# Optimization experiments

Measured on AMD Instinct MI355X. Metric: run time of the kernel, lower is better.

Reference implementation:

```python
import jax, jax.numpy as jnp
import numpy as np

N_HEADS = 16

def setup_inputs() -> dict:
    key = jax.random.key(0)
    ks = jax.random.split(key, 6)
    B, S, D = 2, 2048, 1024
    return {
        "hidden_states": jax.random.normal(ks[0], (B, S, D), dtype=jnp.float32),
        "Wq": jax.random.normal(ks[1], (D, D), dtype=jnp.float32) * (1.0 / np.sqrt(D)),
        "Wk": jax.random.normal(ks[2], (D, D), dtype=jnp.float32) * (1.0 / np.sqrt(D)),
        "Wv": jax.random.normal(ks[3], (D, D), dtype=jnp.float32) * (1.0 / np.sqrt(D)),
        "Wo": jax.random.normal(ks[4], (D, D), dtype=jnp.float32) * (1.0 / np.sqrt(D)),
        "bo": jnp.zeros((D,), dtype=jnp.float32),
    }

def reference(hidden_states, Wq, Wk, Wv, Wo, bo):
    B, S, D = hidden_states.shape
    H = N_HEADS
    hd = D // H  # head_dim; d_kv == d_model per module's final view
    # nn.Linear(bias=False): x @ W.T, then the module's direct view to (B, H, S, hd)
    q = (hidden_states @ Wq.T).reshape(B, H, S, hd)
    k = (hidden_states @ Wk.T).reshape(B, H, S, hd)  # self-attention path (encoder_states=None)
    v = (hidden_states @ Wv.T).reshape(B, H, S, hd)
    # naive full score matrix [B, H, S, S]
    wei = jnp.einsum('bhqd,bhkd->bhqk', q, k)
    causal = jnp.tril(jnp.ones((S, S), dtype=bool))
    wei = jnp.where(causal, wei, -jnp.inf)
    # NOTE: module divides logits by head_dim (not sqrt) -- preserved faithfully
    attn = jax.nn.softmax(wei / hd, axis=-1)
    ctx = jnp.einsum('bhqk,bhkd->bhqd', attn, v)  # [B, H, S, hd]
    out = ctx.transpose(0, 2, 1, 3).reshape(B, S, D)
    return out @ Wo.T + bo
```

## Files before the change

### kernel.cpp

```cpp
#include <hip/hip_runtime.h>

#define S_LEN   2048
#define D_MODEL 1024
#define N_HEADS 16
#define HEAD_DIM 64

typedef unsigned short u16;
typedef float  floatx4 __attribute__((ext_vector_type(4)));
typedef short  bf16x8  __attribute__((ext_vector_type(8)));
typedef short  bf16x4  __attribute__((ext_vector_type(4)));

__device__ __forceinline__ u16 f2bf(float f) {
    unsigned int u = __float_as_uint(f);
    u += 0x7FFF + ((u >> 16) & 1);
    return (u16)(u >> 16);
}
__device__ __forceinline__ unsigned pack2bf(float a, float b) {
    return (unsigned)f2bf(a) | ((unsigned)f2bf(b) << 16);
}

__device__ __forceinline__ void gload_lds16(const void* g, void* l) {
    __builtin_amdgcn_global_load_lds(
        reinterpret_cast<const __attribute__((address_space(1))) unsigned int*>(
            reinterpret_cast<uintptr_t>(g)),
        reinterpret_cast<__attribute__((address_space(3))) unsigned int*>(
            reinterpret_cast<uintptr_t>(l)),
        16, 0, 0);
}

__global__ __launch_bounds__(256) void cast_all(const float* __restrict__ hs,
                                                const float* __restrict__ w0,
                                                const float* __restrict__ w1,
                                                const float* __restrict__ w2,
                                                const float* __restrict__ w3,
                                                u16* __restrict__ dst) {
    const size_t NHS = (size_t)2 * S_LEN * D_MODEL;
    const size_t e0 = (size_t)blockIdx.x * 2048;
    const float* src;
    size_t base;
    if (e0 < NHS)                 { src = hs; base = 0; }
    else {
        const int wi = (int)((e0 - NHS) >> 20);
        src = wi == 0 ? w0 : wi == 1 ? w1 : wi == 2 ? w2 : w3;
        base = NHS + ((size_t)wi << 20);
    }
    const size_t i = e0 + (size_t)threadIdx.x * 8;
    const float4 a = *(const float4*)(src + (i - base));
    const float4 b = *(const float4*)(src + (i - base) + 4);
    uint4 o;
    o.x = pack2bf(a.x, a.y); o.y = pack2bf(a.z, a.w);
    o.z = pack2bf(b.x, b.y); o.w = pack2bf(b.z, b.w);
    *(uint4*)(dst + i) = o;
}

__global__ __launch_bounds__(256) void vtrans(const u16* __restrict__ Vf,
                                              u16* __restrict__ Vt) {
    __shared__ unsigned T[64 * 133];
    const int bh = blockIdx.y;
    const int sBase = blockIdx.x * 128;
    const u16* src = Vf + (size_t)bh * (S_LEN * HEAD_DIM) + (size_t)sBase * HEAD_DIM;
    u16* dst = Vt + (size_t)bh * (S_LEN * HEAD_DIM) + sBase;
    const int tid = threadIdx.x;

#pragma unroll
    for (int it = 0; it < 4; ++it) {
        const int idx = it * 256 + tid;
        const int row = idx >> 3, ch = idx & 7;
        const float4 v4 = *(const float4*)(src + row * 64 + ch * 8);
        const u16* vs = (const u16*)&v4;
#pragma unroll
        for (int j = 0; j < 8; ++j) T[(ch * 8 + j) * 133 + row] = vs[j];
    }
    __syncthreads();
#pragma unroll
    for (int it = 0; it < 4; ++it) {
        const int idx = it * 256 + tid;
        const int d = idx >> 4, sc = idx & 15;
        union { u16 u[8]; float4 f; } tmp;
#pragma unroll
        for (int j = 0; j < 8; ++j) tmp.u[j] = (u16)T[d * 133 + sc * 8 + j];
        *(float4*)(dst + (size_t)d * S_LEN + sc * 8) = tmp.f;
    }
}

__global__ __launch_bounds__(256) void gemm_qkv(const u16* __restrict__ A,
                                                const u16* __restrict__ Wq,
                                                const u16* __restrict__ Wk,
                                                const u16* __restrict__ Wv,
                                                u16* __restrict__ Qo,
                                                u16* __restrict__ Ko,
                                                u16* __restrict__ Vfo) {
    __shared__ u16 As[8 * 512];
    __shared__ u16 Ws[8 * 512];

    const int blk = blockIdx.x;
    const int y   = (blk & 7) | (((blk >> 3) & 3) << 3);
    const int x   = blk >> 5;
    const int which = x >> 3;
    const int nBase = (x & 7) * 128;
    const int mBase = y * 128;
    const u16* W = which == 0 ? Wq : which == 1 ? Wk : Wv;

    const int tid = threadIdx.x, lane = tid & 63, wv = tid >> 6;
    const int l15 = lane & 15, quad = lane >> 4;
    const int wm = wv & 1, wn = wv >> 1;
    const int srow = lane >> 2;
    const int gch  = (lane & 3) ^ ((lane >> 3) & 3);
    const int swz  = (l15 >> 1) & 3;

    floatx4 acc[4][4];
#pragma unroll
    for (int i = 0; i < 4; ++i)
#pragma unroll
        for (int j = 0; j < 4; ++j) acc[i][j] = (floatx4)(0.0f);

    for (int k0 = 0; k0 < D_MODEL; k0 += 32) {
        __syncthreads();
#pragma unroll
        for (int t = 0; t < 2; ++t) {
            const int ci = wv * 2 + t;
            gload_lds16(A + (size_t)(mBase + ci * 16 + srow) * D_MODEL + k0 + gch * 8,
                        &As[ci * 512]);
            gload_lds16(W + (size_t)(nBase + ci * 16 + srow) * D_MODEL + k0 + gch * 8,
                        &Ws[ci * 512]);
        }
        __syncthreads();

        bf16x8 af[4], bfr[4];
#pragma unroll
        for (int mt = 0; mt < 4; ++mt)
            af[mt] = *(const bf16x8*)&As[(wm * 64 + mt * 16 + l15) * 32 + (quad ^ swz) * 8];
#pragma unroll
        for (int nt = 0; nt < 4; ++nt)
            bfr[nt] = *(const bf16x8*)&Ws[(wn * 64 + nt * 16 + l15) * 32 + (quad ^ swz) * 8];
#pragma unroll
        for (int mt = 0; mt < 4; ++mt)
#pragma unroll
            for (int nt = 0; nt < 4; ++nt)
                acc[mt][nt] = __builtin_amdgcn_mfma_f32_16x16x32_bf16(af[mt], bfr[nt], acc[mt][nt], 0, 0, 0);
    }

    u16* O = which == 0 ? Qo : (which == 1 ? Ko : Vfo);
    const float scale = which == 0 ? (1.44269504088896f / 64.0f) : 1.0f;
#pragma unroll
    for (int mt = 0; mt < 4; ++mt)
#pragma unroll
        for (int nt = 0; nt < 4; ++nt) {
            const int col = nBase + wn * 64 + nt * 16 + l15;
#pragma unroll
            for (int r = 0; r < 4; ++r) {
                const int row = mBase + wm * 64 + mt * 16 + quad * 4 + r;
                O[(size_t)row * D_MODEL + col] = f2bf(acc[mt][nt][r] * scale);
            }
        }
}

__global__ __launch_bounds__(256) void gemm_out(const u16* __restrict__ A,
                                                const u16* __restrict__ W,
                                                const float* __restrict__ bias,
                                                float* __restrict__ C) {
    __shared__ u16 As[4 * 512];
    __shared__ u16 Ws[8 * 512];

    const int nBase = blockIdx.x * 128;
    const int mBase = blockIdx.y * 64;
    const int tid = threadIdx.x, lane = tid & 63, wv = tid >> 6;
    const int l15 = lane & 15, quad = lane >> 4;
    const int wm = wv & 1, wn = wv >> 1;
    const int srow = lane >> 2;
    const int gch  = (lane & 3) ^ ((lane >> 3) & 3);
    const int swz  = (l15 >> 1) & 3;

    floatx4 acc[2][4];
#pragma unroll
    for (int i = 0; i < 2; ++i)
#pragma unroll
        for (int j = 0; j < 4; ++j) acc[i][j] = (floatx4)(0.0f);

    for (int k0 = 0; k0 < D_MODEL; k0 += 32) {
        __syncthreads();
        gload_lds16(A + (size_t)(mBase + wv * 16 + srow) * D_MODEL + k0 + gch * 8,
                    &As[wv * 512]);
#pragma unroll
        for (int t = 0; t < 2; ++t) {
            const int ci = wv * 2 + t;
            gload_lds16(W + (size_t)(nBase + ci * 16 + srow) * D_MODEL + k0 + gch * 8,
                        &Ws[ci * 512]);
        }
        __syncthreads();

        bf16x8 af[2], bfr[4];
#pragma unroll
        for (int mt = 0; mt < 2; ++mt)
            af[mt] = *(const bf16x8*)&As[(wm * 32 + mt * 16 + l15) * 32 + (quad ^ swz) * 8];
#pragma unroll
        for (int nt = 0; nt < 4; ++nt)
            bfr[nt] = *(const bf16x8*)&Ws[(wn * 64 + nt * 16 + l15) * 32 + (quad ^ swz) * 8];
#pragma unroll
        for (int mt = 0; mt < 2; ++mt)
#pragma unroll
            for (int nt = 0; nt < 4; ++nt)
                acc[mt][nt] = __builtin_amdgcn_mfma_f32_16x16x32_bf16(af[mt], bfr[nt], acc[mt][nt], 0, 0, 0);
    }

#pragma unroll
    for (int mt = 0; mt < 2; ++mt)
#pragma unroll
        for (int nt = 0; nt < 4; ++nt) {
            const int col = nBase + wn * 64 + nt * 16 + l15;
            const float bv = bias[col];
#pragma unroll
            for (int r = 0; r < 4; ++r) {
                const int row = mBase + wm * 32 + mt * 16 + quad * 4 + r;
                C[(size_t)row * D_MODEL + col] = acc[mt][nt][r] + bv;
            }
        }
}

__global__ __launch_bounds__(256, 3) void attn6(const u16* __restrict__ Q,
                                                const u16* __restrict__ K,
                                                const u16* __restrict__ Vt,
                                                u16* __restrict__ Ctx) {
    __shared__ __align__(16) char smem[35840];
    u16*   Ks    = (u16*)smem;
    u16*   Vs    = (u16*)(smem + 16384);
    float* RedA  = (float*)smem;
    float* RedB  = (float*)(smem + 17408);
    float* lpbuf = (float*)(smem + 34816);

    const int flat = blockIdx.x;
    const int g    = flat & 31;
    const int qt   = 31 - (flat >> 5);
    const int h = g & 15, b = g >> 4;

    const int tid = threadIdx.x, lane = tid & 63, wv = tid >> 6;
    const int l15 = lane & 15, quad = lane >> 4;

    const size_t headOff = ((size_t)b * N_HEADS + h) * S_LEN * HEAD_DIM;
    const u16* Qh = Q + headOff;
    const u16* Kh = K + headOff;
    const u16* Vh = Vt + headOff;
    u16* Cb = Ctx + (size_t)b * S_LEN * D_MODEL + (size_t)h * HEAD_DIM;

    const int srow = lane >> 3;
    const int gch  = (lane & 7) ^ srow;
    const int swz  = l15 & 7;

    const int qBase = qt * 64;

    bf16x8 qb[4][2];
#pragma unroll
    for (int qg = 0; qg < 4; ++qg)
#pragma unroll
        for (int ks = 0; ks < 2; ++ks)
            qb[qg][ks] = *(const bf16x8*)(Qh + (size_t)(qBase + qg * 16 + l15) * 64
                                          + ks * 32 + quad * 8);

    floatx4 o[4][4];
#pragma unroll
    for (int qg = 0; qg < 4; ++qg)
#pragma unroll
        for (int dg = 0; dg < 4; ++dg) o[qg][dg] = (floatx4)(0.0f);
    float lp[4] = {0.0f, 0.0f, 0.0f, 0.0f};

#pragma unroll
    for (int t = 0; t < 2; ++t) {
        const int ci = wv * 2 + t;
        gload_lds16(Kh + (size_t)(ci * 8 + srow) * 64 + gch * 8, &Ks[ci * 512]);
        gload_lds16(Vh + (size_t)(ci * 8 + srow) * S_LEN + gch * 8, &Vs[ci * 512]);
    }
    __syncthreads();

    for (int kt = 0; kt <= qt; ++kt) {
        const int cur = (kt & 1) * 4096;
        const int nxt = 4096 - cur;

        if (kt < qt) {
            const int kB2 = (kt + 1) * 64;
#pragma unroll
            for (int t = 0; t < 2; ++t) {
                const int ci = wv * 2 + t;
                gload_lds16(Kh + (size_t)(kB2 + ci * 8 + srow) * 64 + gch * 8,
                            &Ks[nxt + ci * 512]);
                gload_lds16(Vh + (size_t)(ci * 8 + srow) * S_LEN + kB2 + gch * 8,
                            &Vs[nxt + ci * 512]);
            }
        }

        bf16x8 ka[2];
#pragma unroll
        for (int ks = 0; ks < 2; ++ks)
            ka[ks] = *(const bf16x8*)&Ks[cur + (wv * 16 + l15) * 64 + ((ks * 4 + quad) ^ swz) * 8];

        bf16x4 vb[4];
#pragma unroll
        for (int dg = 0; dg < 4; ++dg)
            vb[dg] = *(const bf16x4*)&Vs[cur + (dg * 16 + l15) * 64
                                         + (((wv * 2 + (quad >> 1)) ^ swz) * 8) + (quad & 1) * 4];

        floatx4 s[4];
#pragma unroll
        for (int qg = 0; qg < 4; ++qg) {
            s[qg] = (floatx4)(0.0f);
#pragma unroll
            for (int ks = 0; ks < 2; ++ks)
                s[qg] = __builtin_amdgcn_mfma_f32_16x16x32_bf16(ka[ks], qb[qg][ks], s[qg], 0, 0, 0);
        }

        const bool diag = (kt == qt);
#pragma unroll
        for (int qg = 0; qg < 4; ++qg) {
            if (diag && qg < wv) continue;
            float p[4];
#pragma unroll
            for (int r = 0; r < 4; ++r) {
                float pv = __builtin_amdgcn_exp2f(s[qg][r]);
                if (diag && qg == wv && (quad * 4 + r > l15)) pv = 0.0f;
                p[r] = pv;
                lp[qg] += pv;
            }
            union { uint2 u; bf16x4 v; } pk;
            pk.u.x = __builtin_amdgcn_perm(__float_as_uint(p[1]), __float_as_uint(p[0]), 0x07060302);
            pk.u.y = __builtin_amdgcn_perm(__float_as_uint(p[3]), __float_as_uint(p[2]), 0x07060302);
#pragma unroll
            for (int dg = 0; dg < 4; ++dg)
                o[qg][dg] = __builtin_amdgcn_mfma_f32_16x16x16bf16_1k(pk.v, vb[dg], o[qg][dg], 0, 0, 0);
        }

        __syncthreads();
    }

#pragma unroll
    for (int qg = 0; qg < 4; ++qg) {
        lp[qg] += __shfl_xor(lp[qg], 16);
        lp[qg] += __shfl_xor(lp[qg], 32);
    }
    lpbuf[wv * 64 + quad * 16 + l15] = lp[quad];

    if (wv == 1 || wv == 3) {
        float* R = (wv == 1) ? RedA : RedB;
#pragma unroll
        for (int qg = 0; qg < 4; ++qg)
#pragma unroll
            for (int dg = 0; dg < 4; ++dg)
                *(floatx4*)&R[(dg * 16 + l15) * 68 + qg * 16 + quad * 4] = o[qg][dg];
    }
    __syncthreads();
    if (wv == 0 || wv == 2) {
        const float* R = (wv == 0) ? RedA : RedB;
#pragma unroll
        for (int qg = 0; qg < 4; ++qg)
#pragma unroll
            for (int dg = 0; dg < 4; ++dg)
                o[qg][dg] += *(const floatx4*)&R[(dg * 16 + l15) * 68 + qg * 16 + quad * 4];
    }
    __syncthreads();
    if (wv == 2) {
#pragma unroll
        for (int qg = 0; qg < 4; ++qg)
#pragma unroll
            for (int dg = 0; dg < 4; ++dg)
                *(floatx4*)&RedA[(dg * 16 + l15) * 68 + qg * 16 + quad * 4] = o[qg][dg];
    }
    __syncthreads();
    if (wv == 0) {
#pragma unroll
        for (int qg = 0; qg < 4; ++qg) {
#pragma unroll
            for (int dg = 0; dg < 4; ++dg)
                o[qg][dg] += *(const floatx4*)&RedA[(dg * 16 + l15) * 68 + qg * 16 + quad * 4];
            floatx4 lt = *(const floatx4*)&lpbuf[0 * 64 + qg * 16 + quad * 4];
            lt += *(const floatx4*)&lpbuf[1 * 64 + qg * 16 + quad * 4];
            lt += *(const floatx4*)&lpbuf[2 * 64 + qg * 16 + quad * 4];
            lt += *(const floatx4*)&lpbuf[3 * 64 + qg * 16 + quad * 4];
#pragma unroll
            for (int r = 0; r < 4; ++r) {
                const float inv = 1.0f / lt[r];
                const int row = qBase + qg * 16 + quad * 4 + r;
#pragma unroll
                for (int dg = 0; dg < 4; ++dg)
                    Cb[(size_t)row * D_MODEL + dg * 16 + l15] = f2bf(o[qg][dg][r] * inv);
            }
        }
    }
}

extern "C" void kernel_launch(void* const* d_in, const int* in_sizes, int n_in,
                              void* d_out, int out_size, void* d_ws, size_t ws_size,
                              hipStream_t stream) {
    const float* hs = (const float*)d_in[0];
    const float* Wq = (const float*)d_in[1];
    const float* Wk = (const float*)d_in[2];
    const float* Wv = (const float*)d_in[3];
    const float* Wo = (const float*)d_in[4];
    const float* bo = (const float*)d_in[5];
    float* out = (float*)d_out;

    const size_t NHS = (size_t)2 * S_LEN * D_MODEL;
    const size_t NW  = (size_t)D_MODEL * D_MODEL;

    u16* hsb = (u16*)d_ws;
    u16* Wb  = hsb + NHS;
    u16* Qb  = Wb + 4 * NW;
    u16* Kb  = Qb + NHS;
    u16* Vfb = Kb + NHS;
    u16* Vtb = Vfb + NHS;
    u16* Cxb = Vtb + NHS;

    cast_all<<<4096, 256, 0, stream>>>(hs, Wq, Wk, Wv, Wo, hsb);

    gemm_qkv<<<768, 256, 0, stream>>>(hsb, Wb, Wb + NW, Wb + 2 * NW,
                                      Qb, Kb, Vfb);

    vtrans<<<dim3(16, 32), 256, 0, stream>>>(Vfb, Vtb);

    attn6<<<1024, 256, 0, stream>>>(Qb, Kb, Vtb, Cxb);

    gemm_out<<<dim3(8, 64), 256, 0, stream>>>(Cxb, Wb + 3 * NW, bo, out);
}
```

Baseline: 168.5 us.

## Fuse all stages into one persistent kernel with grid barriers

Replaces the five separate launches (cast, QKV GEMM, V transpose, attention, output GEMM) with a single persistent kernel of 512 blocks. Stages are separated by a software grid barrier built on atomics in workspace, and the V transpose is overlapped with the second half of the QKV tiles. Attention work is paired so each block takes a long and a short causal tile. This removes launch gaps and tail effects, but adds barrier spin costs and relies on all 512 blocks being co-resident, which risks deadlock if occupancy drops. It also forces the attention code down from 3 to 2 blocks per CU via launch bounds.

```diff
diff --git a/kernel.cpp b/kernel.cpp
--- a/kernel.cpp
+++ b/kernel.cpp
@@ -4,6 +4,7 @@
 #define D_MODEL 1024
 #define N_HEADS 16
 #define HEAD_DIM 64
+#define NBLOCKS 512
 
 typedef unsigned short u16;
 typedef float  floatx4 __attribute__((ext_vector_type(4)));
@@ -28,72 +29,67 @@
         16, 0, 0);
 }
 
-__global__ __launch_bounds__(256) void cast_all(const float* __restrict__ hs,
-                                                const float* __restrict__ w0,
-                                                const float* __restrict__ w1,
-                                                const float* __restrict__ w2,
-                                                const float* __restrict__ w3,
-                                                u16* __restrict__ dst) {
+__device__ __forceinline__ void gridbar(unsigned* bar) {
+    __syncthreads();
+    if (threadIdx.x == 0) {
+        __threadfence();
+        const unsigned gen = __hip_atomic_load(&bar[16], __ATOMIC_ACQUIRE,
+                                               __HIP_MEMORY_SCOPE_AGENT);
+        const unsigned a = __hip_atomic_fetch_add(&bar[0], 1u, __ATOMIC_ACQ_REL,
+                                                  __HIP_MEMORY_SCOPE_AGENT);
+        if (a == NBLOCKS - 1) {
+            __hip_atomic_store(&bar[0], 0u, __ATOMIC_RELAXED,
+                               __HIP_MEMORY_SCOPE_AGENT);
+            __hip_atomic_fetch_add(&bar[16], 1u, __ATOMIC_RELEASE,
+                                   __HIP_MEMORY_SCOPE_AGENT);
+        } else {
+            while (__hip_atomic_load(&bar[16], __ATOMIC_ACQUIRE,
+                                     __HIP_MEMORY_SCOPE_AGENT) == gen)
+                __builtin_amdgcn_s_sleep(8);
+        }
+        __threadfence();
+    }
+    __syncthreads();
+}
+
+__device__ void cast_body(const float* __restrict__ hs,
+                          const float* __restrict__ w0,
+                          const float* __restrict__ w1,
+                          const float* __restrict__ w2,
+                          const float* __restrict__ w3,
+                          u16* __restrict__ dst, int bid) {
     const size_t NHS = (size_t)2 * S_LEN * D_MODEL;
-    const size_t e0 = (size_t)blockIdx.x * 2048;
-    const float* src;
-    size_t base;
-    if (e0 < NHS)                 { src = hs; base = 0; }
-    else {
-        const int wi = (int)((e0 - NHS) >> 20);
-        src = wi == 0 ? w0 : wi == 1 ? w1 : wi == 2 ? w2 : w3;
-        base = NHS + ((size_t)wi << 20);
-    }
-    const size_t i = e0 + (size_t)threadIdx.x * 8;
-    const float4 a = *(const float4*)(src + (i - base));
-    const float4 b = *(const float4*)(src + (i - base) + 4);
-    uint4 o;
-    o.x = pack2bf(a.x, a.y); o.y = pack2bf(a.z, a.w);
-    o.z = pack2bf(b.x, b.y); o.w = pack2bf(b.z, b.w);
-    *(uint4*)(dst + i) = o;
-}
-
-__global__ __launch_bounds__(256) void vtrans(const u16* __restrict__ Vf,
-                                              u16* __restrict__ Vt) {
-    __shared__ unsigned T[64 * 133];
-    const int bh = blockIdx.y;
-    const int sBase = blockIdx.x * 128;
-    const u16* src = Vf + (size_t)bh * (S_LEN * HEAD_DIM) + (size_t)sBase * HEAD_DIM;
-    u16* dst = Vt + (size_t)bh * (S_LEN * HEAD_DIM) + sBase;
-    const int tid = threadIdx.x;
-
-#pragma unroll
-    for (int it = 0; it < 4; ++it) {
-        const int idx = it * 256 + tid;
-        const int row = idx >> 3, ch = idx & 7;
-        const float4 v4 = *(const float4*)(src + row * 64 + ch * 8);
-        const u16* vs = (const u16*)&v4;
-#pragma unroll
-        for (int j = 0; j < 8; ++j) T[(ch * 8 + j) * 133 + row] = vs[j];
-    }
-    __syncthreads();
-#pragma unroll
-    for (int it = 0; it < 4; ++it) {
-        const int idx = it * 256 + tid;
-        const int d = idx >> 4, sc = idx & 15;
-        union { u16 u[8]; float4 f; } tmp;
-#pragma unroll
-        for (int j = 0; j < 8; ++j) tmp.u[j] = (u16)T[d * 133 + sc * 8 + j];
-        *(float4*)(dst + (size_t)d * S_LEN + sc * 8) = tmp.f;
-    }
-}
-
-__global__ __launch_bounds__(256) void gemm_qkv(const u16* __restrict__ A,
-                                                const u16* __restrict__ Wq,
-                                                const u16* __restrict__ Wk,
-                                                const u16* __restrict__ Wv,
-                                                u16* __restrict__ Qo,
-                                                u16* __restrict__ Ko,
-                                                u16* __restrict__ Vfo) {
-    __shared__ u16 As[8 * 512];
-    __shared__ u16 Ws[8 * 512];
-
-    const int blk = blockIdx.x;
+    for (int c = bid; c < 4096; c += NBLOCKS) {
+        const size_t e0 = (size_t)c * 2048;
+        const float* src;
+        size_t base;
+        if (e0 < NHS)                 { src = hs; base = 0; }
+        else {
+            const int wi = (int)((e0 - NHS) >> 20);
+            src = wi == 0 ? w0 : wi == 1 ? w1 : wi == 2 ? w2 : w3;
+            base = NHS + ((size_t)wi << 20);
+        }
+        const size_t i = e0 + (size_t)threadIdx.x * 8;
+        const float4 a = *(const float4*)(src + (i - base));
+        const float4 b = *(const float4*)(src + (i - base) + 4);
+        uint4 o;
+        o.x = pack2bf(a.x, a.y); o.y = pack2bf(a.z, a.w);
+        o.z = pack2bf(b.x, b.y); o.w = pack2bf(b.z, b.w);
+        *(uint4*)(dst + i) = o;
+    }
+}
+
+__device__ void qkv_tile(const u16* __restrict__ A,
+                         const u16* __restrict__ Wq,
+                         const u16* __restrict__ Wk,
+                         const u16* __restrict__ Wv,
+                         u16* __restrict__ Qo,
+                         u16* __restrict__ Ko,
+                         u16* __restrict__ Vfo,
+                         char* smem, int blk) {
+    u16* As = (u16*)smem;
+    u16* Ws = (u16*)(smem + 8192);
+
     const int y   = (blk & 7) | (((blk >> 3) & 3) << 3);
     const int x   = blk >> 5;
     const int which = x >> 3;
@@ -153,82 +149,52 @@
                 O[(size_t)row * D_MODEL + col] = f2bf(acc[mt][nt][r] * scale);
             }
         }
-}
-
-__global__ __launch_bounds__(256) void gemm_out(const u16* __restrict__ A,
-                                                const u16* __restrict__ W,
-                                                const float* __restrict__ bias,
-                                                float* __restrict__ C) {
-    __shared__ u16 As[4 * 512];
-    __shared__ u16 Ws[8 * 512];
-
-    const int nBase = blockIdx.x * 128;
-    const int mBase = blockIdx.y * 64;
-    const int tid = threadIdx.x, lane = tid & 63, wv = tid >> 6;
-    const int l15 = lane & 15, quad = lane >> 4;
-    const int wm = wv & 1, wn = wv >> 1;
-    const int srow = lane >> 2;
-    const int gch  = (lane & 3) ^ ((lane >> 3) & 3);
-    const int swz  = (l15 >> 1) & 3;
-
-    floatx4 acc[2][4];
-#pragma unroll
-    for (int i = 0; i < 2; ++i)
-#pragma unroll
-        for (int j = 0; j < 4; ++j) acc[i][j] = (floatx4)(0.0f);
-
-    for (int k0 = 0; k0 < D_MODEL; k0 += 32) {
-        __syncthreads();
-        gload_lds16(A + (size_t)(mBase + wv * 16 + srow) * D_MODEL + k0 + gch * 8,
-                    &As[wv * 512]);
-#pragma unroll
-        for (int t = 0; t < 2; ++t) {
-            const int ci = wv * 2 + t;
-            gload_lds16(W + (size_t)(nBase + ci * 16 + srow) * D_MODEL + k0 + gch * 8,
-                        &Ws[ci * 512]);
-        }
-        __syncthreads();
-
-        bf16x8 af[2], bfr[4];
-#pragma unroll
-        for (int mt = 0; mt < 2; ++mt)
-            af[mt] = *(const bf16x8*)&As[(wm * 32 + mt * 16 + l15) * 32 + (quad ^ swz) * 8];
-#pragma unroll
-        for (int nt = 0; nt < 4; ++nt)
-            bfr[nt] = *(const bf16x8*)&Ws[(wn * 64 + nt * 16 + l15) * 32 + (quad ^ swz) * 8];
-#pragma unroll
-        for (int mt = 0; mt < 2; ++mt)
-#pragma unroll
-            for (int nt = 0; nt < 4; ++nt)
-                acc[mt][nt] = __builtin_amdgcn_mfma_f32_16x16x32_bf16(af[mt], bfr[nt], acc[mt][nt], 0, 0, 0);
-    }
-
-#pragma unroll
-    for (int mt = 0; mt < 2; ++mt)
-#pragma unroll
-        for (int nt = 0; nt < 4; ++nt) {
-            const int col = nBase + wn * 64 + nt * 16 + l15;
-            const float bv = bias[col];
-#pragma unroll
-            for (int r = 0; r < 4; ++r) {
-                const int row = mBase + wm * 32 + mt * 16 + quad * 4 + r;
-                C[(size_t)row * D_MODEL + col] = acc[mt][nt][r] + bv;
-            }
-        }
-}
-
-__global__ __launch_bounds__(256, 3) void attn6(const u16* __restrict__ Q,
-                                                const u16* __restrict__ K,
-                                                const u16* __restrict__ Vt,
-                                                u16* __restrict__ Ctx) {
-    __shared__ __align__(16) char smem[35840];
+    __syncthreads();
+}
+
+__device__ void vtrans_body(const u16* __restrict__ Vf,
+                            u16* __restrict__ Vt,
+                            char* smem, int v) {
+    unsigned* T = (unsigned*)smem;
+    const int bh = v >> 4;
+    const int sBase = (v & 15) * 128;
+    const u16* src = Vf + (size_t)bh * (S_LEN * HEAD_DIM) + (size_t)sBase * HEAD_DIM;
+    u16* dst = Vt + (size_t)bh * (S_LEN * HEAD_DIM) + sBase;
+    const int tid = threadIdx.x;
+
+#pragma unroll
+    for (int it = 0; it < 4; ++it) {
+        const int idx = it * 256 + tid;
+        const int row = idx >> 3, ch = idx & 7;
+        const float4 v4 = *(const float4*)(src + row * 64 + ch * 8);
+        const u16* vs = (const u16*)&v4;
+#pragma unroll
+        for (int j = 0; j < 8; ++j) T[(ch * 8 + j) * 133 + row] = vs[j];
+    }
+    __syncthreads();
+#pragma unroll
+    for (int it = 0; it < 4; ++it) {
+        const int idx = it * 256 + tid;
+        const int d = idx >> 4, sc = idx & 15;
+        union { u16 u[8]; float4 f; } tmp;
+#pragma unroll
+        for (int j = 0; j < 8; ++j) tmp.u[j] = (u16)T[d * 133 + sc * 8 + j];
+        *(float4*)(dst + (size_t)d * S_LEN + sc * 8) = tmp.f;
+    }
+    __syncthreads();
+}
+
+__device__ void attn_task(const u16* __restrict__ Q,
+                          const u16* __restrict__ K,
+                          const u16* __restrict__ Vt,
+                          u16* __restrict__ Ctx,
+                          char* smem, int flat) {
     u16*   Ks    = (u16*)smem;
     u16*   Vs    = (u16*)(smem + 16384);
     float* RedA  = (float*)smem;
     float* RedB  = (float*)(smem + 17408);
     float* lpbuf = (float*)(smem + 34816);
 
-    const int flat = blockIdx.x;
     const int g    = flat & 31;
     const int qt   = 31 - (flat >> 5);
     const int h = g & 15, b = g >> 4;
@@ -383,6 +349,116 @@
             }
         }
     }
+    __syncthreads();
+}
+
+__device__ void out_body(const u16* __restrict__ A,
+                         const u16* __restrict__ W,
+                         const float* __restrict__ bias,
+                         float* __restrict__ C,
+                         char* smem, int o) {
+    u16* As = (u16*)smem;
+    u16* Ws = (u16*)(smem + 4096);
+
+    const int nBase = (o & 7) * 128;
+    const int mBase = (o >> 3) * 64;
+    const int tid = threadIdx.x, lane = tid & 63, wv = tid >> 6;
+    const int l15 = lane & 15, quad = lane >> 4;
+    const int wm = wv & 1, wn = wv >> 1;
+    const int srow = lane >> 2;
+    const int gch  = (lane & 3) ^ ((lane >> 3) & 3);
+    const int swz  = (l15 >> 1) & 3;
+
+    floatx4 acc[2][4];
+#pragma unroll
+    for (int i = 0; i < 2; ++i)
+#pragma unroll
+        for (int j = 0; j < 4; ++j) acc[i][j] = (floatx4)(0.0f);
+
+    for (int k0 = 0; k0 < D_MODEL; k0 += 32) {
+        __syncthreads();
+        gload_lds16(A + (size_t)(mBase + wv * 16 + srow) * D_MODEL + k0 + gch * 8,
+                    &As[wv * 512]);
+#pragma unroll
+        for (int t = 0; t < 2; ++t) {
+            const int ci = wv * 2 + t;
+            gload_lds16(W + (size_t)(nBase + ci * 16 + srow) * D_MODEL + k0 + gch * 8,
+                        &Ws[ci * 512]);
+        }
+        __syncthreads();
+
+        bf16x8 af[2], bfr[4];
+#pragma unroll
+        for (int mt = 0; mt < 2; ++mt)
+            af[mt] = *(const bf16x8*)&As[(wm * 32 + mt * 16 + l15) * 32 + (quad ^ swz) * 8];
+#pragma unroll
+        for (int nt = 0; nt < 4; ++nt)
+            bfr[nt] = *(const bf16x8*)&Ws[(wn * 64 + nt * 16 + l15) * 32 + (quad ^ swz) * 8];
+#pragma unroll
+        for (int mt = 0; mt < 2; ++mt)
+#pragma unroll
+            for (int nt = 0; nt < 4; ++nt)
+                acc[mt][nt] = __builtin_amdgcn_mfma_f32_16x16x32_bf16(af[mt], bfr[nt], acc[mt][nt], 0, 0, 0);
+    }
+
+#pragma unroll
+    for (int mt = 0; mt < 2; ++mt)
+#pragma unroll
+        for (int nt = 0; nt < 4; ++nt) {
+            const int col = nBase + wn * 64 + nt * 16 + l15;
+            const float bv = bias[col];
+#pragma unroll
+            for (int r = 0; r < 4; ++r) {
+                const int row = mBase + wm * 32 + mt * 16 + quad * 4 + r;
+                C[(size_t)row * D_MODEL + col] = acc[mt][nt][r] + bv;
+            }
+        }
+}
+
+__global__ __launch_bounds__(256, 2) void mega(const float* __restrict__ hs,
+                                               const float* __restrict__ Wqf,
+                                               const float* __restrict__ Wkf,
+                                               const float* __restrict__ Wvf,
+                                               const float* __restrict__ Wof,
+                                               const float* __restrict__ bo,
+                                               float* __restrict__ out,
+                                               u16* __restrict__ ws) {
+    __shared__ __align__(16) char smem[35840];
+    const int bid = blockIdx.x;
+
+    const size_t NHS = (size_t)2 * S_LEN * D_MODEL;
+    const size_t NW  = (size_t)D_MODEL * D_MODEL;
+    u16* hsb = ws;
+    u16* Wb  = hsb + NHS;
+    u16* Qb  = Wb + 4 * NW;
+    u16* Kb  = Qb + NHS;
+    u16* Vfb = Kb + NHS;
+    u16* Vtb = Vfb + NHS;
+    u16* Cxb = Vtb + NHS;
+    unsigned* bar = (unsigned*)((char*)ws + ((size_t)64 << 20));
+
+    cast_body(hs, Wqf, Wkf, Wvf, Wof, hsb, bid);
+    gridbar(bar);
+
+    {
+        const int t1 = (bid < 256) ? bid : bid + 256;
+        qkv_tile(hsb, Wb, Wb + NW, Wb + 2 * NW, Qb, Kb, Vfb, smem, t1);
+    }
+    gridbar(bar);
+
+    if (bid < 256) {
+        qkv_tile(hsb, Wb, Wb + NW, Wb + 2 * NW, Qb, Kb, Vfb, smem, bid + 256);
+    } else {
+        vtrans_body(Vfb, Vtb, smem, (bid - 256) * 2);
+        vtrans_body(Vfb, Vtb, smem, (bid - 256) * 2 + 1);
+    }
+    gridbar(bar);
+
+    attn_task(Qb, Kb, Vtb, Cxb, smem, bid);
+    attn_task(Qb, Kb, Vtb, Cxb, smem, 1023 - bid);
+    gridbar(bar);
+
+    out_body(Cxb, Wb + 3 * NW, bo, out, smem, bid);
 }
 
 extern "C" void kernel_launch(void* const* d_in, const int* in_sizes, int n_in,
@@ -395,26 +471,9 @@
     const float* Wo = (const float*)d_in[4];
     const float* bo = (const float*)d_in[5];
     float* out = (float*)d_out;
-
-    const size_t NHS = (size_t)2 * S_LEN * D_MODEL;
-    const size_t NW  = (size_t)D_MODEL * D_MODEL;
-
-    u16* hsb = (u16*)d_ws;
-    u16* Wb  = hsb + NHS;
-    u16* Qb  = Wb + 4 * NW;
-    u16* Kb  = Qb + NHS;
-    u16* Vfb = Kb + NHS;
-    u16* Vtb = Vfb + NHS;
-    u16* Cxb = Vtb + NHS;
-
-    cast_all<<<4096, 256, 0, stream>>>(hs, Wq, Wk, Wv, Wo, hsb);
-
-    gemm_qkv<<<768, 256, 0, stream>>>(hsb, Wb, Wb + NW, Wb + 2 * NW,
-                                      Qb, Kb, Vfb);
-
-    vtrans<<<dim3(16, 32), 256, 0, stream>>>(Vfb, Vtb);
-
-    attn6<<<1024, 256, 0, stream>>>(Qb, Kb, Vtb, Cxb);
-
-    gemm_out<<<dim3(8, 64), 256, 0, stream>>>(Cxb, Wb + 3 * NW, bo, out);
-}
+    u16* ws = (u16*)d_ws;
+
+    hipMemsetAsync((char*)d_ws + ((size_t)64 << 20), 0, 256, stream);
+
+    mega<<<NBLOCKS, 256, 0, stream>>>(hs, Wq, Wk, Wv, Wo, bo, out, ws);
+}
```

Result: slower. 632.9 us (+275.7%).
